# Kernel optimization log

Measured on AMD Instinct MI355X. Metric: run time of the kernel, lower is better.

Reference implementation:

```python
import jax, jax.numpy as jnp
import numpy as np

EPS = 1e-5

def conv1x1(x, w):
    # x: [B,C,H,W], w: [O,C] -> [B,O,H,W]
    return jnp.einsum('oc,bchw->bohw', w, x)

def bn(x, g, b, m, v):
    # inference batchnorm over channel dim 1
    scale = g / jnp.sqrt(v + EPS)
    return x * scale[None, :, None, None] + (b - m * scale)[None, :, None, None]

def setup_inputs() -> dict:
    key = jax.random.key(0)
    ks = jax.random.split(key, 20)
    B, Cin, S = 32, 256, 32
    C = Cin // 2
    rn = lambda k, sh: jax.random.normal(k, sh, dtype=jnp.float32)
    ru = lambda k, sh: jax.random.uniform(k, sh, dtype=jnp.float32)
    return {
        'x': rn(ks[0], (B, Cin, S, S)),
        'w1': rn(ks[1], (C, Cin)) * 0.05,
        'bn1_g': ru(ks[2], (C,)) + 0.5,
        'bn1_b': rn(ks[3], (C,)) * 0.1,
        'bn1_m': rn(ks[4], (C,)) * 0.1,
        'bn1_v': ru(ks[5], (C,)) + 0.5,
        'wq': rn(ks[6], (C, C)) * 0.05,
        'bq': rn(ks[7], (C,)) * 0.05,
        'wk': rn(ks[8], (C, C)) * 0.05,
        'bk': rn(ks[9], (C,)) * 0.05,
        'wv': rn(ks[10], (C, C)) * 0.05,
        'bv': rn(ks[11], (C,)) * 0.05,
        'rel_h': rn(ks[12], (1, C, S, 1)),
        'rel_w': rn(ks[13], (1, C, 1, S)),
        'w2': rn(ks[14], (Cin, C)) * 0.05,
        'bn2_g': ru(ks[15], (Cin,)) + 0.5,
        'bn2_b': rn(ks[16], (Cin,)) * 0.1,
        'bn2_m': rn(ks[17], (Cin,)) * 0.1,
        'bn2_v': ru(ks[18], (Cin,)) + 0.5,
    }

def reference(x, w1, bn1_g, bn1_b, bn1_m, bn1_v, wq, bq, wk, bk, wv, bv,
              rel_h, rel_w, w2, bn2_g, bn2_b, bn2_m, bn2_v):
    # cv1: 1x1 conv -> BN -> SiLU
    x1 = jax.nn.silu(bn(conv1x1(x, w1), bn1_g, bn1_b, bn1_m, bn1_v))
    B, C, H, W = x1.shape
    N = H * W
    # q/k/v: 1x1 conv with bias, flattened to [B,C,N]
    q = (conv1x1(x1, wq) + bq[None, :, None, None]).reshape(B, C, N)
    k = (conv1x1(x1, wk) + bk[None, :, None, None]).reshape(B, C, N)
    v = (conv1x1(x1, wv) + bv[None, :, None, None]).reshape(B, C, N)
    # content-content: q^T k -> [B,N,N]
    content_content = jnp.einsum('bci,bcj->bij', q, k)
    # content-position: pos^T q -> [B,N,N]
    pos = (rel_h + rel_w).reshape(C, N)  # [C,N]
    content_position = jnp.einsum('ci,bcj->bij', pos, q)
    attention = jax.nn.softmax(content_content + content_position, axis=-1)
    # out[b,c,i] = sum_j v[b,c,j] * attention[b,i,j]
    out = jnp.einsum('bcj,bij->bci', v, attention).reshape(B, C, H, W)
    # cv2: 1x1 conv -> BN -> SiLU, plus residual shortcut
    y = jax.nn.silu(bn(conv1x1(out, w2), bn2_g, bn2_b, bn2_m, bn2_v))
    return x + y
```

## Files before the change

### kernel.cpp

```cpp
#include <hip/hip_runtime.h>
#include <stdint.h>

typedef __bf16 bf16x8 __attribute__((ext_vector_type(8)));
typedef float  f32x4  __attribute__((ext_vector_type(4)));
typedef float  f32x16 __attribute__((ext_vector_type(16)));

#define MFMA(a,b,c)   __builtin_amdgcn_mfma_f32_16x16x32_bf16((a),(b),(c),0,0,0)
#define MFMA32(a,b,c) __builtin_amdgcn_mfma_f32_32x32x16_bf16((a),(b),(c),0,0,0)

__device__ __forceinline__ short f2b(float x) {
  uint32_t u = __float_as_uint(x);
  uint32_t r = (u + 0x7fffu + ((u >> 16) & 1u)) >> 16;
  return (short)r;
}

__device__ __forceinline__ uint32_t cvtpk(float lo, float hi) {
  uint32_t w;
  asm("v_cvt_pk_bf16_f32 %0, %1, %2" : "=v"(w) : "v"(lo), "v"(hi));
  return w;
}

__device__ __forceinline__ void glds16(const void* g, void* l) {
  __builtin_amdgcn_global_load_lds(
      (const __attribute__((address_space(1))) void*)(uintptr_t)g,
      (__attribute__((address_space(3))) void*)(uintptr_t)l, 16, 0, 0);
}

__global__ void k_prep(const float* __restrict__ w1, const float* __restrict__ wq,
                       const float* __restrict__ wk, const float* __restrict__ wv,
                       const float* __restrict__ w2,
                       const float* __restrict__ relh, const float* __restrict__ relw,
                       const float* __restrict__ g1, const float* __restrict__ b1,
                       const float* __restrict__ m1, const float* __restrict__ v1,
                       const float* __restrict__ g2, const float* __restrict__ b2,
                       const float* __restrict__ m2, const float* __restrict__ v2,
                       short* __restrict__ w1b, short* __restrict__ wqb,
                       short* __restrict__ wkb, short* __restrict__ wvb,
                       short* __restrict__ w2b, short* __restrict__ posT,
                       float* __restrict__ bnc) {
  int i = blockIdx.x * 256 + threadIdx.x;
  if (i < 32768) { w1b[i] = f2b(w1[i]); return; }
  i -= 32768;
  if (i < 16384) { wqb[i] = f2b(wq[i]); return; }
  i -= 16384;
  if (i < 16384) { wkb[i] = f2b(wk[i]); return; }
  i -= 16384;
  if (i < 16384) { wvb[i] = f2b(wv[i]); return; }
  i -= 16384;
  if (i < 32768) { w2b[i] = f2b(w2[i]); return; }
  i -= 32768;
  if (i < 131072) {
    int n = i >> 7, c = i & 127;
    int h = n >> 5, w = n & 31;
    posT[i] = f2b(relh[c * 32 + h] + relw[c * 32 + w]);
    return;
  }
  i -= 131072;
  if (i < 128) { float s = g1[i] * rsqrtf(v1[i] + 1e-5f); bnc[i] = s; bnc[128 + i] = b1[i] - m1[i] * s; return; }
  i -= 128;
  if (i < 256) { float s = g2[i] * rsqrtf(v2[i] + 1e-5f); bnc[256 + i] = s; bnc[512 + i] = b2[i] - m2[i] * s; return; }
}

__launch_bounds__(256)
__global__ void k_cq(const float* __restrict__ x, const short* __restrict__ w1b,
                     const short* __restrict__ wqb, const short* __restrict__ wkb,
                     const short* __restrict__ wvb, const float* __restrict__ bnc,
                     const float* __restrict__ bq, const float* __restrict__ bk,
                     const float* __restrict__ bv,
                     short* __restrict__ qT, short* __restrict__ kT,
                     short* __restrict__ vv) {
  __shared__ __align__(16) short Al[128 * 40];
  __shared__ __align__(16) short Bl[128 * 40];
  __shared__ __align__(16) short X1[128 * 136];
  const int bx = blockIdx.x;
  const int b = bx >> 3;
  const int n0 = (bx & 7) << 7;
  const int tid = threadIdx.x;
  const int wid = tid >> 6, lane = tid & 63;
  const int wr = wid >> 1, wc = wid & 1;
  const int cpr = lane & 15, g = lane >> 4;
  const float* xb = x + (size_t)b * (256 * 1024);

  {
    f32x4 acc[4][4] = {};
    for (int kk = 0; kk < 8; ++kk) {
#pragma unroll
      for (int it = 0; it < 2; ++it) {
        int f = tid + it * 256;
        int row = f >> 2, c8 = f & 3;
        *reinterpret_cast<uint4*>(&Al[row * 40 + c8 * 8]) =
            *reinterpret_cast<const uint4*>(&w1b[row * 256 + kk * 32 + c8 * 8]);
      }
#pragma unroll
      for (int it = 0; it < 4; ++it) {
        int f = tid + it * 256;
        int ci = f >> 5, c4 = f & 31;
        float4 v4 = *reinterpret_cast<const float4*>(&xb[(size_t)(kk * 32 + ci) * 1024 + n0 + c4 * 4]);
        int nb = c4 * 4;
        Bl[(nb + 0) * 40 + ci] = f2b(v4.x);
        Bl[(nb + 1) * 40 + ci] = f2b(v4.y);
        Bl[(nb + 2) * 40 + ci] = f2b(v4.z);
        Bl[(nb + 3) * 40 + ci] = f2b(v4.w);
      }
      __syncthreads();
      bf16x8 af[4], bfr[4];
#pragma unroll
      for (int mf = 0; mf < 4; ++mf)
        af[mf] = *reinterpret_cast<const bf16x8*>(&Al[(wr * 64 + mf * 16 + cpr) * 40 + g * 8]);
#pragma unroll
      for (int nf = 0; nf < 4; ++nf)
        bfr[nf] = *reinterpret_cast<const bf16x8*>(&Bl[(wc * 64 + nf * 16 + cpr) * 40 + g * 8]);
#pragma unroll
      for (int mf = 0; mf < 4; ++mf)
#pragma unroll
        for (int nf = 0; nf < 4; ++nf)
          acc[mf][nf] = MFMA(af[mf], bfr[nf], acc[mf][nf]);
      __syncthreads();
    }
#pragma unroll
    for (int mf = 0; mf < 4; ++mf) {
      int m0 = wr * 64 + mf * 16 + g * 4;
#pragma unroll
      for (int nf = 0; nf < 4; ++nf) {
        int nl = wc * 64 + nf * 16 + cpr;
        union { short s[4]; uint2 u; } pk;
#pragma unroll
        for (int r = 0; r < 4; ++r) {
          int c = m0 + r;
          float z = acc[mf][nf][r] * bnc[c] + bnc[128 + c];
          pk.s[r] = f2b(z / (1.f + __expf(-z)));
        }
        *reinterpret_cast<uint2*>(&X1[nl * 136 + m0]) = pk.u;
      }
    }
  }
  __syncthreads();

  for (int which = 0; which < 3; ++which) {
    const short* W = which == 0 ? wqb : which == 1 ? wkb : wvb;
    const float* bias = which == 0 ? bq : which == 1 ? bk : bv;
    f32x4 acc[4][4] = {};
    for (int kk = 0; kk < 4; ++kk) {
#pragma unroll
      for (int it = 0; it < 2; ++it) {
        int f = tid + it * 256;
        int row = f >> 2, c8 = f & 3;
        *reinterpret_cast<uint4*>(&Al[row * 40 + c8 * 8]) =
            *reinterpret_cast<const uint4*>(&W[row * 128 + kk * 32 + c8 * 8]);
      }
      __syncthreads();
      bf16x8 af[4], bfr[4];
#pragma unroll
      for (int mf = 0; mf < 4; ++mf)
        af[mf] = *reinterpret_cast<const bf16x8*>(&Al[(wr * 64 + mf * 16 + cpr) * 40 + g * 8]);
#pragma unroll
      for (int nf = 0; nf < 4; ++nf)
        bfr[nf] = *reinterpret_cast<const bf16x8*>(&X1[(wc * 64 + nf * 16 + cpr) * 136 + kk * 32 + g * 8]);
#pragma unroll
      for (int mf = 0; mf < 4; ++mf)
#pragma unroll
        for (int nf = 0; nf < 4; ++nf)
          acc[mf][nf] = MFMA(af[mf], bfr[nf], acc[mf][nf]);
      __syncthreads();
    }
#pragma unroll
    for (int mf = 0; mf < 4; ++mf) {
      int m0 = wr * 64 + mf * 16 + g * 4;
#pragma unroll
      for (int nf = 0; nf < 4; ++nf) {
        int n = n0 + wc * 64 + nf * 16 + cpr;
        if (which < 2) {
          union { short s4[4]; uint2 u; } pk;
#pragma unroll
          for (int r = 0; r < 4; ++r)
            pk.s4[r] = f2b(acc[mf][nf][r] + bias[m0 + r]);
          short* dst = which == 0 ? qT : kT;
          *reinterpret_cast<uint2*>(&dst[((size_t)b * 1024 + n) * 128 + m0]) = pk.u;
        } else {
#pragma unroll
          for (int r = 0; r < 4; ++r) {
            int c = m0 + r;
            vv[((size_t)b * 128 + c) * 1024 + n] = f2b(acc[mf][nf][r] + bias[c]);
          }
        }
      }
    }
  }
}

__launch_bounds__(512, 1)
__global__ void k_attn(const short* __restrict__ qT, const short* __restrict__ kT,
                       const short* __restrict__ vv, const short* __restrict__ posT,
                       const short* __restrict__ w2b, const float* __restrict__ bnc,
                       const float* __restrict__ x, float* __restrict__ out) {
  __shared__ __align__(16) char smem[100864];
  short* KhB0 = (short*)smem;
  short* KhB1 = (short*)(smem + 32768);
  short* VtB0 = (short*)(smem + 65536);
  short* VtB1 = (short*)(smem + 65536 + 16384);
  float*    Obuf  = (float*)smem;
  uint16_t* ObufB = (uint16_t*)(smem + 66048);
  float*    mlf   = (float*)(smem + 98816);

  const int bx0 = blockIdx.x;
  const int lbx = ((bx0 & 7) << 5) | (bx0 >> 3);
  const int b  = lbx >> 3;
  const int i0 = (lbx & 7) << 7;
  const int tid = threadIdx.x;
  const int wid = tid >> 6, lane = tid & 63;
  const int rl = lane & 31, hi = lane >> 5;
  const int jh = wid >> 2, iq = wid & 3;
  const size_t bN = (size_t)b * 1024;

  const short* srcK[4];
  const short* srcV[2];
#pragma unroll
  for (int it = 0; it < 4; ++it) {
    int gq = it * 512 + tid;
    int row = gq >> 5, p = gq & 31;
    int l = p ^ (row & 7);
    srcK[it] = (l < 16) ? &kT[(bN + row) * 128 + l * 8]
                        : &qT[(bN + row) * 128 + (l - 16) * 8];
  }
#pragma unroll
  for (int it = 0; it < 2; ++it) {
    int gq = it * 512 + tid;
    int c = gq >> 3, p = gq & 7;
    int l = p ^ (c & 7);
    srcV[it] = &vv[((size_t)b * 128 + c) * 1024 + l * 8];
  }
#pragma unroll
  for (int it = 0; it < 4; ++it) glds16(srcK[it], &KhB0[(it * 512 + wid * 64) * 8]);
#pragma unroll
  for (int it = 0; it < 2; ++it) glds16(srcV[it], &VtB0[(it * 512 + wid * 64) * 8]);

  bf16x8 qf[16];
  {
    const int irow = i0 + iq * 32 + rl;
#pragma unroll
    for (int ks = 0; ks < 8; ++ks)
      qf[ks] = *reinterpret_cast<const bf16x8*>(&qT[(bN + irow) * 128 + ks * 16 + hi * 8]);
#pragma unroll
    for (int ks = 8; ks < 16; ++ks)
      qf[ks] = *reinterpret_cast<const bf16x8*>(&posT[(size_t)irow * 128 + (ks - 8) * 16 + hi * 8]);
  }
  __syncthreads();

  f32x16 oacc[4] = {};
  float mrow = -3e38f, lrow = 0.f;

  for (int jt = 0; jt < 16; ++jt) {
    const int cur = jt & 1;
    if (jt < 15) {
      short* KhN = cur ? KhB0 : KhB1;
      short* VtN = cur ? VtB0 : VtB1;
#pragma unroll
      for (int it = 0; it < 4; ++it)
        glds16(srcK[it] + ((jt + 1) << 13), &KhN[(it * 512 + wid * 64) * 8]);
#pragma unroll
      for (int it = 0; it < 2; ++it)
        glds16(srcV[it] + ((jt + 1) << 6), &VtN[(it * 512 + wid * 64) * 8]);
    }
    const short* KhC = cur ? KhB1 : KhB0;
    const short* VtC = cur ? VtB1 : VtB0;

    f32x16 s0 = {}, s1 = {};
    {
      const int rb = (jh * 32 + rl) * 256;
      __builtin_amdgcn_s_setprio(1);
#pragma unroll
      for (int ks = 0; ks < 16; ++ks) {
        int p = ((ks << 1) | hi) ^ (rl & 7);
        bf16x8 kf = *reinterpret_cast<const bf16x8*>(&KhC[rb + p * 8]);
        if (ks & 1) s1 = MFMA32(kf, qf[ks], s1);
        else        s0 = MFMA32(kf, qf[ks], s0);
      }
      __builtin_amdgcn_s_setprio(0);
    }
    float t[16];
#pragma unroll
    for (int r = 0; r < 16; ++r) t[r] = s0[r] + s1[r];
    float mx = t[0];
#pragma unroll
    for (int r = 1; r < 16; ++r) mx = fmaxf(mx, t[r]);
    mx = fmaxf(mx, __shfl_xor(mx, 32));
    float pr[16];
    float ps = 0.f;
    if (__all(mx <= mrow + 8.f)) {
#pragma unroll
      for (int r = 0; r < 16; ++r) { pr[r] = __expf(t[r] - mrow); ps += pr[r]; }
      ps += __shfl_xor(ps, 32);
      lrow += ps;
    } else {
      float mnew = fmaxf(mrow, mx);
      float sc = __expf(mrow - mnew);
#pragma unroll
      for (int r = 0; r < 16; ++r) { pr[r] = __expf(t[r] - mnew); ps += pr[r]; }
      ps += __shfl_xor(ps, 32);
      lrow = lrow * sc + ps;
      mrow = mnew;
#pragma unroll
      for (int ct = 0; ct < 4; ++ct)
#pragma unroll
        for (int r = 0; r < 16; ++r) oacc[ct][r] *= sc;
    }
    uint32_t own[8], rcv[8];
#pragma unroll
    for (int idx = 0; idx < 8; ++idx) own[idx] = cvtpk(pr[2 * idx], pr[2 * idx + 1]);
#pragma unroll
    for (int idx = 0; idx < 8; ++idx) rcv[idx] = __shfl_xor((int)own[idx], 32);
#pragma unroll
    for (int js = 0; js < 2; ++js) {
      union { uint32_t u[4]; bf16x8 v; } pa;
      pa.u[0] = hi ? rcv[4 * js + 2] : own[4 * js + 0];
      pa.u[1] = hi ? rcv[4 * js + 3] : own[4 * js + 1];
      pa.u[2] = hi ? own[4 * js + 2] : rcv[4 * js + 0];
      pa.u[3] = hi ? own[4 * js + 3] : rcv[4 * js + 1];
      __builtin_amdgcn_s_setprio(1);
#pragma unroll
      for (int ct = 0; ct < 4; ++ct) {
        int c = ct * 32 + rl;
        int p = ((jh << 2) | (js << 1) | hi) ^ (rl & 7);
        bf16x8 vf = *reinterpret_cast<const bf16x8*>(&VtC[c * 64 + p * 8]);
        oacc[ct] = MFMA32(vf, pa.v, oacc[ct]);
      }
      __builtin_amdgcn_s_setprio(0);
    }
    __syncthreads();
  }

  if (lane < 32) {
    mlf[wid * 64 + rl]      = mrow;
    mlf[wid * 64 + 32 + rl] = lrow;
  }
  __syncthreads();
  float scl;
  {
    const int pid = wid ^ 4;
    float mp = mlf[pid * 64 + rl];
    float lp = mlf[pid * 64 + 32 + rl];
    float M  = fmaxf(mrow, mp);
    float f  = __expf(mrow - M);
    float fp = __expf(mp - M);
    scl = f / (lrow * f + lp * fp);
  }
  bf16x8 af2[8];
#pragma unroll
  for (int ks = 0; ks < 8; ++ks)
    af2[ks] = *reinterpret_cast<const bf16x8*>(&w2b[(size_t)(wid * 32 + rl) * 128 + ks * 16 + hi * 8]);
  __syncthreads();

  const int row = iq * 32 + rl;
  if (jh == 0) {
#pragma unroll
    for (int ct = 0; ct < 4; ++ct)
#pragma unroll
      for (int r = 0; r < 16; ++r) {
        int c = ct * 32 + (r & 3) + 8 * (r >> 2) + 4 * hi;
        Obuf[row * 129 + c] = oacc[ct][r] * scl;
      }
  }
  __syncthreads();
  if (jh == 1) {
    uint32_t* OW = (uint32_t*)ObufB;
#pragma unroll
    for (int ct = 0; ct < 4; ++ct) {
      float mg[16];
#pragma unroll
      for (int r = 0; r < 16; ++r) {
        int c = ct * 32 + (r & 3) + 8 * (r >> 2) + 4 * hi;
        mg[r] = Obuf[row * 129 + c] + oacc[ct][r] * scl;
      }
#pragma unroll
      for (int m = 0; m < 8; ++m) {
        int c0 = ct * 32 + ((2 * m) & 3) + 8 * ((2 * m) >> 2) + 4 * hi;
        int gI = c0 >> 3, wo = (c0 & 7) >> 1;
        int gS = gI ^ (row & 15);
        OW[row * 64 + gS * 4 + wo] = cvtpk(mg[2 * m], mg[2 * m + 1]);
      }
    }
  }
  __syncthreads();

  f32x16 a2[4] = {};
#pragma unroll
  for (int it = 0; it < 4; ++it) {
    const int r2 = it * 32 + rl;
    __builtin_amdgcn_s_setprio(1);
#pragma unroll
    for (int ks = 0; ks < 8; ++ks) {
      int gS = ((ks << 1) | hi) ^ (r2 & 15);
      bf16x8 bf = *reinterpret_cast<const bf16x8*>(&ObufB[r2 * 128 + gS * 8]);
      a2[it] = MFMA32(af2[ks], bf, a2[it]);
    }
    __builtin_amdgcn_s_setprio(0);
  }
  float bsc[16], bsh[16];
#pragma unroll
  for (int r = 0; r < 16; ++r) {
    int co = wid * 32 + (r & 3) + 8 * (r >> 2) + 4 * hi;
    bsc[r] = bnc[256 + co];
    bsh[r] = bnc[512 + co];
  }
#pragma unroll
  for (int it = 0; it < 4; ++it) {
#pragma unroll
    for (int r = 0; r < 16; ++r) {
      int co = wid * 32 + (r & 3) + 8 * (r >> 2) + 4 * hi;
      size_t idx = ((size_t)b * 256 + co) * 1024 + i0 + it * 32 + rl;
      float y = a2[it][r] * bsc[r] + bsh[r];
      out[idx] = x[idx] + y / (1.f + __expf(-y));
    }
  }
}

extern "C" void kernel_launch(void* const* d_in, const int* in_sizes, int n_in,
                              void* d_out, int out_size, void* d_ws, size_t ws_size,
                              hipStream_t stream) {
  (void)in_sizes; (void)n_in; (void)out_size; (void)ws_size;
  const float* x    = (const float*)d_in[0];
  const float* w1   = (const float*)d_in[1];
  const float* g1   = (const float*)d_in[2];
  const float* b1   = (const float*)d_in[3];
  const float* m1   = (const float*)d_in[4];
  const float* v1   = (const float*)d_in[5];
  const float* wq   = (const float*)d_in[6];
  const float* bq   = (const float*)d_in[7];
  const float* wk   = (const float*)d_in[8];
  const float* bk   = (const float*)d_in[9];
  const float* wv   = (const float*)d_in[10];
  const float* bv   = (const float*)d_in[11];
  const float* relh = (const float*)d_in[12];
  const float* relw = (const float*)d_in[13];
  const float* w2   = (const float*)d_in[14];
  const float* g2   = (const float*)d_in[15];
  const float* b2   = (const float*)d_in[16];
  const float* m2   = (const float*)d_in[17];
  const float* v2   = (const float*)d_in[18];
  float* out = (float*)d_out;

  char* ws = (char*)d_ws;
  const size_t OFF_W1B  = 0;
  const size_t OFF_WQB  = 65536;
  const size_t OFF_WKB  = 98304;
  const size_t OFF_WVB  = 131072;
  const size_t OFF_W2B  = 163840;
  const size_t OFF_POST = 229376;
  const size_t OFF_BN   = 491520;
  const size_t OFF_QT   = 494592;
  const size_t OFF_KT   = OFF_QT + 8388608;
  const size_t OFF_V    = OFF_KT + 8388608;

  short* w1b  = (short*)(ws + OFF_W1B);
  short* wqb  = (short*)(ws + OFF_WQB);
  short* wkb  = (short*)(ws + OFF_WKB);
  short* wvb  = (short*)(ws + OFF_WVB);
  short* w2b  = (short*)(ws + OFF_W2B);
  short* posT = (short*)(ws + OFF_POST);
  float* bnc  = (float*)(ws + OFF_BN);
  short* qT   = (short*)(ws + OFF_QT);
  short* kT   = (short*)(ws + OFF_KT);
  short* vv   = (short*)(ws + OFF_V);

  k_prep<<<962, 256, 0, stream>>>(w1, wq, wk, wv, w2, relh, relw,
                                  g1, b1, m1, v1, g2, b2, m2, v2,
                                  w1b, wqb, wkb, wvb, w2b, posT, bnc);
  k_cq<<<256, 256, 0, stream>>>(x, w1b, wqb, wkb, wvb, bnc, bq, bk, bv, qT, kT, vv);
  k_attn<<<256, 512, 0, stream>>>(qT, kT, vv, posT, w2b, bnc, x, out);
}
```

Measured before the change: 97.13 us.

## Halve attention tile to 64 queries, run two blocks per CU with register-staged V

The attention kernel now uses 256-thread blocks that each own 64 query rows, launching 512 blocks with two resident per CU instead of one 512-thread block per CU. K tiles are prefetched two steps ahead through direct global-to-LDS loads. V tiles are staged through registers into a single LDS buffer, with explicit waitcnt and barrier control in place of __syncthreads. The output projection is split so each wave computes 64 output channels. The aim is better latency hiding and overlap through higher occupancy and deeper prefetch, at the cost of more register pressure and duplicated K/V traffic, since each batch's K/V is now read by 16 blocks instead of 8.

```diff
diff --git a/kernel.cpp b/kernel.cpp
--- a/kernel.cpp
+++ b/kernel.cpp
@@ -188,52 +188,56 @@
   }
 }
 
-__launch_bounds__(512, 1)
+__launch_bounds__(256, 2)
 __global__ void k_attn(const short* __restrict__ qT, const short* __restrict__ kT,
                        const short* __restrict__ vv, const short* __restrict__ posT,
                        const short* __restrict__ w2b, const float* __restrict__ bnc,
                        const float* __restrict__ x, float* __restrict__ out) {
-  __shared__ __align__(16) char smem[100864];
-  short* KhB0 = (short*)smem;
-  short* KhB1 = (short*)(smem + 32768);
-  short* VtB0 = (short*)(smem + 65536);
-  short* VtB1 = (short*)(smem + 65536 + 16384);
+  __shared__ __align__(16) char smem[81920];
+  short* Kh0 = (short*)smem;
+  short* Kh1 = (short*)(smem + 32768);
+  short* Vt  = (short*)(smem + 65536);
   float*    Obuf  = (float*)smem;
-  uint16_t* ObufB = (uint16_t*)(smem + 66048);
-  float*    mlf   = (float*)(smem + 98816);
+  uint16_t* ObufB = (uint16_t*)(smem + 33024);
+  float*    mlf   = (float*)(smem + 49408);
 
   const int bx0 = blockIdx.x;
-  const int lbx = ((bx0 & 7) << 5) | (bx0 >> 3);
-  const int b  = lbx >> 3;
-  const int i0 = (lbx & 7) << 7;
+  const int lbx = ((bx0 & 7) << 6) | (bx0 >> 3);
+  const int b  = lbx >> 4;
+  const int i0 = (lbx & 15) << 6;
   const int tid = threadIdx.x;
   const int wid = tid >> 6, lane = tid & 63;
   const int rl = lane & 31, hi = lane >> 5;
-  const int jh = wid >> 2, iq = wid & 3;
+  const int jh = wid >> 1, iq = wid & 1;
   const size_t bN = (size_t)b * 1024;
 
-  const short* srcK[4];
-  const short* srcV[2];
-#pragma unroll
-  for (int it = 0; it < 4; ++it) {
-    int gq = it * 512 + tid;
+  const short* srcK[8];
+#pragma unroll
+  for (int it = 0; it < 8; ++it) {
+    int gq = it * 256 + tid;
     int row = gq >> 5, p = gq & 31;
     int l = p ^ (row & 7);
     srcK[it] = (l < 16) ? &kT[(bN + row) * 128 + l * 8]
                         : &qT[(bN + row) * 128 + (l - 16) * 8];
   }
-#pragma unroll
-  for (int it = 0; it < 2; ++it) {
-    int gq = it * 512 + tid;
-    int c = gq >> 3, p = gq & 7;
-    int l = p ^ (c & 7);
-    srcV[it] = &vv[((size_t)b * 128 + c) * 1024 + l * 8];
-  }
-#pragma unroll
-  for (int it = 0; it < 4; ++it) glds16(srcK[it], &KhB0[(it * 512 + wid * 64) * 8]);
-#pragma unroll
-  for (int it = 0; it < 2; ++it) glds16(srcV[it], &VtB0[(it * 512 + wid * 64) * 8]);
-
+  const short* srcVg[4];
+#pragma unroll
+  for (int it = 0; it < 4; ++it) {
+    int gq = it * 256 + tid;
+    int c = gq >> 3, pd = gq & 7;
+    int l = pd ^ (c & 7);
+    srcVg[it] = &vv[((size_t)b * 128 + c) * 1024 + l * 8];
+  }
+
+  uint4 vreg[4];
+#pragma unroll
+  for (int it = 0; it < 4; ++it) vreg[it] = *reinterpret_cast<const uint4*>(srcVg[it]);
+  __builtin_amdgcn_sched_barrier(0);
+#pragma unroll
+  for (int it = 0; it < 8; ++it) glds16(srcK[it], &Kh0[(it * 256 + wid * 64) * 8]);
+#pragma unroll
+  for (int it = 0; it < 8; ++it) glds16(srcK[it] + (1 << 13), &Kh1[(it * 256 + wid * 64) * 8]);
+  __builtin_amdgcn_sched_barrier(0);
   bf16x8 qf[16];
   {
     const int irow = i0 + iq * 32 + rl;
@@ -244,26 +248,28 @@
     for (int ks = 8; ks < 16; ++ks)
       qf[ks] = *reinterpret_cast<const bf16x8*>(&posT[(size_t)irow * 128 + (ks - 8) * 16 + hi * 8]);
   }
-  __syncthreads();
+  __builtin_amdgcn_sched_barrier(0);
+#pragma unroll
+  for (int it = 0; it < 4; ++it) {
+    int gq = it * 256 + tid;
+    int c = gq >> 3, pd = gq & 7;
+    *reinterpret_cast<uint4*>(&Vt[c * 64 + pd * 8]) = vreg[it];
+  }
+  __builtin_amdgcn_sched_barrier(0);
+#pragma unroll
+  for (int it = 0; it < 4; ++it) vreg[it] = *reinterpret_cast<const uint4*>(srcVg[it] + 64);
+  __builtin_amdgcn_sched_barrier(0);
+  asm volatile("s_waitcnt vmcnt(4)" ::: "memory");
+  __builtin_amdgcn_sched_barrier(0);
+  asm volatile("s_waitcnt lgkmcnt(0)" ::: "memory");
+  __builtin_amdgcn_sched_barrier(0);
+  asm volatile("s_barrier" ::: "memory");
 
   f32x16 oacc[4] = {};
   float mrow = -3e38f, lrow = 0.f;
 
   for (int jt = 0; jt < 16; ++jt) {
-    const int cur = jt & 1;
-    if (jt < 15) {
-      short* KhN = cur ? KhB0 : KhB1;
-      short* VtN = cur ? VtB0 : VtB1;
-#pragma unroll
-      for (int it = 0; it < 4; ++it)
-        glds16(srcK[it] + ((jt + 1) << 13), &KhN[(it * 512 + wid * 64) * 8]);
-#pragma unroll
-      for (int it = 0; it < 2; ++it)
-        glds16(srcV[it] + ((jt + 1) << 6), &VtN[(it * 512 + wid * 64) * 8]);
-    }
-    const short* KhC = cur ? KhB1 : KhB0;
-    const short* VtC = cur ? VtB1 : VtB0;
-
+    const short* KhC = (jt & 1) ? Kh1 : Kh0;
     f32x16 s0 = {}, s1 = {};
     {
       const int rb = (jh * 32 + rl) * 256;
@@ -321,12 +327,39 @@
       for (int ct = 0; ct < 4; ++ct) {
         int c = ct * 32 + rl;
         int p = ((jh << 2) | (js << 1) | hi) ^ (rl & 7);
-        bf16x8 vf = *reinterpret_cast<const bf16x8*>(&VtC[c * 64 + p * 8]);
+        bf16x8 vf = *reinterpret_cast<const bf16x8*>(&Vt[c * 64 + p * 8]);
         oacc[ct] = MFMA32(vf, pa.v, oacc[ct]);
       }
       __builtin_amdgcn_s_setprio(0);
     }
-    __syncthreads();
+    asm volatile("s_barrier" ::: "memory");
+    if (jt < 15) {
+#pragma unroll
+      for (int it = 0; it < 4; ++it) {
+        int gq = it * 256 + tid;
+        int c = gq >> 3, pd = gq & 7;
+        *reinterpret_cast<uint4*>(&Vt[c * 64 + pd * 8]) = vreg[it];
+      }
+      __builtin_amdgcn_sched_barrier(0);
+      if (jt < 14) {
+#pragma unroll
+        for (int it = 0; it < 4; ++it)
+          vreg[it] = *reinterpret_cast<const uint4*>(srcVg[it] + ((jt + 2) << 6));
+        __builtin_amdgcn_sched_barrier(0);
+        short* KhN = (jt & 1) ? Kh1 : Kh0;
+#pragma unroll
+        for (int it = 0; it < 8; ++it)
+          glds16(srcK[it] + ((size_t)(jt + 2) << 13), &KhN[(it * 256 + wid * 64) * 8]);
+        __builtin_amdgcn_sched_barrier(0);
+        asm volatile("s_waitcnt vmcnt(12)" ::: "memory");
+      } else {
+        asm volatile("s_waitcnt vmcnt(0)" ::: "memory");
+      }
+      __builtin_amdgcn_sched_barrier(0);
+      asm volatile("s_waitcnt lgkmcnt(0)" ::: "memory");
+      __builtin_amdgcn_sched_barrier(0);
+      asm volatile("s_barrier" ::: "memory");
+    }
   }
 
   if (lane < 32) {
@@ -336,7 +369,7 @@
   __syncthreads();
   float scl;
   {
-    const int pid = wid ^ 4;
+    const int pid = wid ^ 2;
     float mp = mlf[pid * 64 + rl];
     float lp = mlf[pid * 64 + 32 + rl];
     float M  = fmaxf(mrow, mp);
@@ -344,10 +377,13 @@
     float fp = __expf(mp - M);
     scl = f / (lrow * f + lp * fp);
   }
-  bf16x8 af2[8];
-#pragma unroll
-  for (int ks = 0; ks < 8; ++ks)
-    af2[ks] = *reinterpret_cast<const bf16x8*>(&w2b[(size_t)(wid * 32 + rl) * 128 + ks * 16 + hi * 8]);
+  bf16x8 af2[2][8];
+#pragma unroll
+  for (int sub = 0; sub < 2; ++sub)
+#pragma unroll
+    for (int ks = 0; ks < 8; ++ks)
+      af2[sub][ks] = *reinterpret_cast<const bf16x8*>(
+          &w2b[(size_t)(wid * 64 + sub * 32 + rl) * 128 + ks * 16 + hi * 8]);
   __syncthreads();
 
   const int row = iq * 32 + rl;
@@ -382,34 +418,38 @@
   }
   __syncthreads();
 
-  f32x16 a2[4] = {};
-#pragma unroll
-  for (int it = 0; it < 4; ++it) {
+  f32x16 a2[2][2] = {};
+#pragma unroll
+  for (int it = 0; it < 2; ++it) {
     const int r2 = it * 32 + rl;
     __builtin_amdgcn_s_setprio(1);
 #pragma unroll
     for (int ks = 0; ks < 8; ++ks) {
       int gS = ((ks << 1) | hi) ^ (r2 & 15);
       bf16x8 bf = *reinterpret_cast<const bf16x8*>(&ObufB[r2 * 128 + gS * 8]);
-      a2[it] = MFMA32(af2[ks], bf, a2[it]);
+      a2[0][it] = MFMA32(af2[0][ks], bf, a2[0][it]);
+      a2[1][it] = MFMA32(af2[1][ks], bf, a2[1][it]);
     }
     __builtin_amdgcn_s_setprio(0);
   }
-  float bsc[16], bsh[16];
-#pragma unroll
-  for (int r = 0; r < 16; ++r) {
-    int co = wid * 32 + (r & 3) + 8 * (r >> 2) + 4 * hi;
-    bsc[r] = bnc[256 + co];
-    bsh[r] = bnc[512 + co];
-  }
-#pragma unroll
-  for (int it = 0; it < 4; ++it) {
+#pragma unroll
+  for (int sub = 0; sub < 2; ++sub) {
+    float bsc[16], bsh[16];
 #pragma unroll
     for (int r = 0; r < 16; ++r) {
-      int co = wid * 32 + (r & 3) + 8 * (r >> 2) + 4 * hi;
-      size_t idx = ((size_t)b * 256 + co) * 1024 + i0 + it * 32 + rl;
-      float y = a2[it][r] * bsc[r] + bsh[r];
-      out[idx] = x[idx] + y / (1.f + __expf(-y));
+      int co = wid * 64 + sub * 32 + (r & 3) + 8 * (r >> 2) + 4 * hi;
+      bsc[r] = bnc[256 + co];
+      bsh[r] = bnc[512 + co];
+    }
+#pragma unroll
+    for (int it = 0; it < 2; ++it) {
+#pragma unroll
+      for (int r = 0; r < 16; ++r) {
+        int co = wid * 64 + sub * 32 + (r & 3) + 8 * (r >> 2) + 4 * hi;
+        size_t idx = ((size_t)b * 256 + co) * 1024 + i0 + it * 32 + rl;
+        float y = a2[sub][it][r] * bsc[r] + bsh[r];
+        out[idx] = x[idx] + y / (1.f + __expf(-y));
+      }
     }
   }
 }
@@ -466,5 +506,5 @@
                                   g1, b1, m1, v1, g2, b2, m2, v2,
                                   w1b, wqb, wkb, wvb, w2b, posT, bnc);
   k_cq<<<256, 256, 0, stream>>>(x, w1b, wqb, wkb, wvb, bnc, bq, bk, bv, qT, kT, vv);
-  k_attn<<<256, 512, 0, stream>>>(qT, kT, vv, posT, w2b, bnc, x, out);
-}
+  k_attn<<<512, 256, 0, stream>>>(qT, kT, vv, posT, w2b, bnc, x, out);
+}
```

Measured after the change: 148.6 us. 53.0% more time.

## Software-pipeline QK^T one tile ahead of softmax/PV and prefetch residual x

Applied to the files above, without the earlier changes.

The attention loop now computes the QK^T scores for tile j+1 while running softmax and PV on tile j. K tiles are loaded two steps ahead and V one step ahead, using ping-pong score accumulators and an unrolled macro. The residual x values are loaded before the final conv GEMM so their latency overlaps the MFMAs. Launch bounds change to request 2 blocks per CU, which tightens the register budget and may cause spills; with about 100KB of LDS per block, actual occupancy may not rise.

```diff
diff --git a/kernel.cpp b/kernel.cpp
--- a/kernel.cpp
+++ b/kernel.cpp
@@ -188,16 +188,16 @@
   }
 }
 
-__launch_bounds__(512, 1)
+__launch_bounds__(512, 2)
 __global__ void k_attn(const short* __restrict__ qT, const short* __restrict__ kT,
                        const short* __restrict__ vv, const short* __restrict__ posT,
                        const short* __restrict__ w2b, const float* __restrict__ bnc,
                        const float* __restrict__ x, float* __restrict__ out) {
   __shared__ __align__(16) char smem[100864];
-  short* KhB0 = (short*)smem;
-  short* KhB1 = (short*)(smem + 32768);
-  short* VtB0 = (short*)(smem + 65536);
-  short* VtB1 = (short*)(smem + 65536 + 16384);
+  short* Kh0 = (short*)smem;
+  short* Kh1 = (short*)(smem + 32768);
+  short* Vt0 = (short*)(smem + 65536);
+  short* Vt1 = (short*)(smem + 65536 + 16384);
   float*    Obuf  = (float*)smem;
   uint16_t* ObufB = (uint16_t*)(smem + 66048);
   float*    mlf   = (float*)(smem + 98816);
@@ -230,9 +230,11 @@
     srcV[it] = &vv[((size_t)b * 128 + c) * 1024 + l * 8];
   }
 #pragma unroll
-  for (int it = 0; it < 4; ++it) glds16(srcK[it], &KhB0[(it * 512 + wid * 64) * 8]);
-#pragma unroll
-  for (int it = 0; it < 2; ++it) glds16(srcV[it], &VtB0[(it * 512 + wid * 64) * 8]);
+  for (int it = 0; it < 4; ++it) glds16(srcK[it], &Kh0[(it * 512 + wid * 64) * 8]);
+#pragma unroll
+  for (int it = 0; it < 4; ++it) glds16(srcK[it] + (1 << 13), &Kh1[(it * 512 + wid * 64) * 8]);
+#pragma unroll
+  for (int it = 0; it < 2; ++it) glds16(srcV[it], &Vt0[(it * 512 + wid * 64) * 8]);
 
   bf16x8 qf[16];
   {
@@ -248,86 +250,98 @@
 
   f32x16 oacc[4] = {};
   float mrow = -3e38f, lrow = 0.f;
-
-  for (int jt = 0; jt < 16; ++jt) {
-    const int cur = jt & 1;
-    if (jt < 15) {
-      short* KhN = cur ? KhB0 : KhB1;
-      short* VtN = cur ? VtB0 : VtB1;
-#pragma unroll
-      for (int it = 0; it < 4; ++it)
-        glds16(srcK[it] + ((jt + 1) << 13), &KhN[(it * 512 + wid * 64) * 8]);
-#pragma unroll
-      for (int it = 0; it < 2; ++it)
-        glds16(srcV[it] + ((jt + 1) << 6), &VtN[(it * 512 + wid * 64) * 8]);
-    }
-    const short* KhC = cur ? KhB1 : KhB0;
-    const short* VtC = cur ? VtB1 : VtB0;
-
-    f32x16 s0 = {}, s1 = {};
-    {
-      const int rb = (jh * 32 + rl) * 256;
-      __builtin_amdgcn_s_setprio(1);
-#pragma unroll
-      for (int ks = 0; ks < 16; ++ks) {
-        int p = ((ks << 1) | hi) ^ (rl & 7);
-        bf16x8 kf = *reinterpret_cast<const bf16x8*>(&KhC[rb + p * 8]);
-        if (ks & 1) s1 = MFMA32(kf, qf[ks], s1);
-        else        s0 = MFMA32(kf, qf[ks], s0);
-      }
-      __builtin_amdgcn_s_setprio(0);
-    }
-    float t[16];
-#pragma unroll
-    for (int r = 0; r < 16; ++r) t[r] = s0[r] + s1[r];
-    float mx = t[0];
-#pragma unroll
-    for (int r = 1; r < 16; ++r) mx = fmaxf(mx, t[r]);
-    mx = fmaxf(mx, __shfl_xor(mx, 32));
-    float pr[16];
-    float ps = 0.f;
-    if (__all(mx <= mrow + 8.f)) {
-#pragma unroll
-      for (int r = 0; r < 16; ++r) { pr[r] = __expf(t[r] - mrow); ps += pr[r]; }
-      ps += __shfl_xor(ps, 32);
-      lrow += ps;
-    } else {
-      float mnew = fmaxf(mrow, mx);
-      float sc = __expf(mrow - mnew);
-#pragma unroll
-      for (int r = 0; r < 16; ++r) { pr[r] = __expf(t[r] - mnew); ps += pr[r]; }
-      ps += __shfl_xor(ps, 32);
-      lrow = lrow * sc + ps;
-      mrow = mnew;
-#pragma unroll
-      for (int ct = 0; ct < 4; ++ct)
-#pragma unroll
-        for (int r = 0; r < 16; ++r) oacc[ct][r] *= sc;
-    }
-    uint32_t own[8], rcv[8];
-#pragma unroll
-    for (int idx = 0; idx < 8; ++idx) own[idx] = cvtpk(pr[2 * idx], pr[2 * idx + 1]);
-#pragma unroll
-    for (int idx = 0; idx < 8; ++idx) rcv[idx] = __shfl_xor((int)own[idx], 32);
-#pragma unroll
-    for (int js = 0; js < 2; ++js) {
-      union { uint32_t u[4]; bf16x8 v; } pa;
-      pa.u[0] = hi ? rcv[4 * js + 2] : own[4 * js + 0];
-      pa.u[1] = hi ? rcv[4 * js + 3] : own[4 * js + 1];
-      pa.u[2] = hi ? own[4 * js + 2] : rcv[4 * js + 0];
-      pa.u[3] = hi ? own[4 * js + 3] : rcv[4 * js + 1];
-      __builtin_amdgcn_s_setprio(1);
-#pragma unroll
-      for (int ct = 0; ct < 4; ++ct) {
-        int c = ct * 32 + rl;
-        int p = ((jh << 2) | (js << 1) | hi) ^ (rl & 7);
-        bf16x8 vf = *reinterpret_cast<const bf16x8*>(&VtC[c * 64 + p * 8]);
-        oacc[ct] = MFMA32(vf, pa.v, oacc[ct]);
-      }
-      __builtin_amdgcn_s_setprio(0);
-    }
-    __syncthreads();
-  }
+  const int rb = (jh * 32 + rl) * 256;
+
+  f32x16 sA = {}, sB = {};
+  {
+    __builtin_amdgcn_s_setprio(1);
+#pragma unroll
+    for (int ks = 0; ks < 16; ++ks) {
+      int p = ((ks << 1) | hi) ^ (rl & 7);
+      bf16x8 kf = *reinterpret_cast<const bf16x8*>(&Kh0[rb + p * 8]);
+      sA = MFMA32(kf, qf[ks], sA);
+    }
+    __builtin_amdgcn_s_setprio(0);
+  }
+  __syncthreads();
+
+#define STEP(JT, SP, SC, KH_OVW, KH_NXT, VT_CUR, VT_NXT)                          \
+  {                                                                               \
+    const int jt_ = (JT);                                                         \
+    if (jt_ < 15) {                                                               \
+      _Pragma("unroll")                                                           \
+      for (int it = 0; it < 2; ++it)                                              \
+        glds16(srcV[it] + ((jt_ + 1) << 6), &VT_NXT[(it * 512 + wid * 64) * 8]);  \
+      if (jt_ < 14) {                                                             \
+        _Pragma("unroll")                                                         \
+        for (int it = 0; it < 4; ++it)                                            \
+          glds16(srcK[it] + ((size_t)(jt_ + 2) << 13),                            \
+                 &KH_OVW[(it * 512 + wid * 64) * 8]);                             \
+      }                                                                           \
+      SC = (f32x16){};                                                            \
+      __builtin_amdgcn_s_setprio(1);                                              \
+      _Pragma("unroll")                                                           \
+      for (int ks = 0; ks < 16; ++ks) {                                           \
+        int p = ((ks << 1) | hi) ^ (rl & 7);                                      \
+        bf16x8 kf = *reinterpret_cast<const bf16x8*>(&KH_NXT[rb + p * 8]);        \
+        SC = MFMA32(kf, qf[ks], SC);                                              \
+      }                                                                           \
+      __builtin_amdgcn_s_setprio(0);                                              \
+    }                                                                             \
+    float mx = SP[0];                                                             \
+    _Pragma("unroll")                                                             \
+    for (int r = 1; r < 16; ++r) mx = fmaxf(mx, SP[r]);                           \
+    mx = fmaxf(mx, __shfl_xor(mx, 32));                                           \
+    float pr[16];                                                                 \
+    float ps = 0.f;                                                               \
+    if (__all(mx <= mrow + 8.f)) {                                                \
+      _Pragma("unroll")                                                           \
+      for (int r = 0; r < 16; ++r) { pr[r] = __expf(SP[r] - mrow); ps += pr[r]; } \
+      ps += __shfl_xor(ps, 32);                                                   \
+      lrow += ps;                                                                 \
+    } else {                                                                      \
+      float mnew = fmaxf(mrow, mx);                                               \
+      float sc = __expf(mrow - mnew);                                             \
+      _Pragma("unroll")                                                           \
+      for (int r = 0; r < 16; ++r) { pr[r] = __expf(SP[r] - mnew); ps += pr[r]; } \
+      ps += __shfl_xor(ps, 32);                                                   \
+      lrow = lrow * sc + ps;                                                      \
+      mrow = mnew;                                                                \
+      _Pragma("unroll")                                                           \
+      for (int ct = 0; ct < 4; ++ct)                                              \
+        _Pragma("unroll")                                                         \
+        for (int r = 0; r < 16; ++r) oacc[ct][r] *= sc;                           \
+    }                                                                             \
+    uint32_t own[8], rcv[8];                                                      \
+    _Pragma("unroll")                                                             \
+    for (int idx = 0; idx < 8; ++idx) own[idx] = cvtpk(pr[2 * idx], pr[2 * idx + 1]); \
+    _Pragma("unroll")                                                             \
+    for (int idx = 0; idx < 8; ++idx) rcv[idx] = __shfl_xor((int)own[idx], 32);   \
+    _Pragma("unroll")                                                             \
+    for (int js = 0; js < 2; ++js) {                                              \
+      union { uint32_t u[4]; bf16x8 v; } pa;                                      \
+      pa.u[0] = hi ? rcv[4 * js + 2] : own[4 * js + 0];                           \
+      pa.u[1] = hi ? rcv[4 * js + 3] : own[4 * js + 1];                           \
+      pa.u[2] = hi ? own[4 * js + 2] : rcv[4 * js + 0];                           \
+      pa.u[3] = hi ? own[4 * js + 3] : rcv[4 * js + 1];                           \
+      __builtin_amdgcn_s_setprio(1);                                              \
+      _Pragma("unroll")                                                           \
+      for (int ct = 0; ct < 4; ++ct) {                                            \
+        int c = ct * 32 + rl;                                                     \
+        int p = ((jh << 2) | (js << 1) | hi) ^ (rl & 7);                          \
+        bf16x8 vf = *reinterpret_cast<const bf16x8*>(&VT_CUR[c * 64 + p * 8]);    \
+        oacc[ct] = MFMA32(vf, pa.v, oacc[ct]);                                    \
+      }                                                                           \
+      __builtin_amdgcn_s_setprio(0);                                              \
+    }                                                                             \
+    __syncthreads();                                                              \
+  }
+
+  for (int jp = 0; jp < 8; ++jp) {
+    STEP(2 * jp,     sA, sB, Kh0, Kh1, Vt0, Vt1);
+    STEP(2 * jp + 1, sB, sA, Kh1, Kh0, Vt1, Vt0);
+  }
+#undef STEP
 
   if (lane < 32) {
     mlf[wid * 64 + rl]      = mrow;
@@ -382,6 +396,16 @@
   }
   __syncthreads();
 
+  float xp0[16], xp1[16], xp2[16], xp3[16];
+#pragma unroll
+  for (int r = 0; r < 16; ++r) {
+    int co = wid * 32 + (r & 3) + 8 * (r >> 2) + 4 * hi;
+    size_t base = ((size_t)b * 256 + co) * 1024 + i0 + rl;
+    xp0[r] = x[base];
+    xp1[r] = x[base + 32];
+    xp2[r] = x[base + 64];
+    xp3[r] = x[base + 96];
+  }
   f32x16 a2[4] = {};
 #pragma unroll
   for (int it = 0; it < 4; ++it) {
@@ -403,14 +427,17 @@
     bsh[r] = bnc[512 + co];
   }
 #pragma unroll
-  for (int it = 0; it < 4; ++it) {
-#pragma unroll
-    for (int r = 0; r < 16; ++r) {
-      int co = wid * 32 + (r & 3) + 8 * (r >> 2) + 4 * hi;
-      size_t idx = ((size_t)b * 256 + co) * 1024 + i0 + it * 32 + rl;
-      float y = a2[it][r] * bsc[r] + bsh[r];
-      out[idx] = x[idx] + y / (1.f + __expf(-y));
-    }
+  for (int r = 0; r < 16; ++r) {
+    int co = wid * 32 + (r & 3) + 8 * (r >> 2) + 4 * hi;
+    size_t base = ((size_t)b * 256 + co) * 1024 + i0 + rl;
+    float y0 = a2[0][r] * bsc[r] + bsh[r];
+    float y1 = a2[1][r] * bsc[r] + bsh[r];
+    float y2 = a2[2][r] * bsc[r] + bsh[r];
+    float y3 = a2[3][r] * bsc[r] + bsh[r];
+    out[base]      = xp0[r] + y0 / (1.f + __expf(-y0));
+    out[base + 32] = xp1[r] + y1 / (1.f + __expf(-y1));
+    out[base + 64] = xp2[r] + y2 / (1.f + __expf(-y2));
+    out[base + 96] = xp3[r] + y3 / (1.f + __expf(-y3));
   }
 }
 
```

Result: slower. 136.9 us (+40.9%).
